# Kernel tuning notes

Measured on AMD Instinct MI355X. Metric: run time of the kernel, lower is better.

Reference implementation:

```python
import jax, jax.numpy as jnp
import numpy as np

N = 50000        # nodes
E = 800000       # directed edges (before self loops)
G = 1024         # graphs in batch
D = 128          # embedding_dim
H = 4            # attention heads
L = 3            # num_layers
NODE_DIM = 78
SLOPE = 0.2      # PyG GATConv leaky_relu negative slope
EPS = 1e-16


def setup_inputs() -> dict:
    key = jax.random.key(0)
    ks = jax.random.split(key, 20)
    s = lambda *sh: 1.0 / np.sqrt(sh[0])
    inp = {
        "x": jax.random.normal(ks[0], (N, NODE_DIM), jnp.float32),
        "edge_index": jax.random.randint(ks[1], (2, E), 0, N, jnp.int64),
        "batch": jnp.sort(jax.random.randint(ks[2], (N,), 0, G, jnp.int64)),
        # node_linear: Linear(78,128) -> ReLU -> Linear(128,128)
        "W1": jax.random.normal(ks[3], (NODE_DIM, D), jnp.float32) * s(NODE_DIM),
        "b1": jnp.zeros((D,), jnp.float32),
        "W2": jax.random.normal(ks[4], (D, D), jnp.float32) * s(D),
        "b2": jnp.zeros((D,), jnp.float32),
        # L stacked GATConv(D, D, heads=H, concat=False)
        "lin_w": jax.random.normal(ks[5], (L, D, H, D), jnp.float32) * s(D),
        "att_src": jax.random.normal(ks[6], (L, H, D), jnp.float32) * s(D),
        "att_dst": jax.random.normal(ks[7], (L, H, D), jnp.float32) * s(D),
        "conv_b": jnp.zeros((L, D), jnp.float32),
        # global_fc: Linear(128,1024) -> ReLU -> Dropout -> Linear(1024,128)
        "gW1": jax.random.normal(ks[8], (D, 1024), jnp.float32) * s(D),
        "gb1": jnp.zeros((1024,), jnp.float32),
        "gW2": jax.random.normal(ks[9], (1024, D), jnp.float32) * s(1024),
        "gb2": jnp.zeros((D,), jnp.float32),
    }
    return inp


def _gat_layer(x, src, dst, W, a_src, a_dst, b):
    # x: [N, D]; W: [D, H, D]
    h = jnp.einsum('nd,dhe->nhe', x, W)                    # [N, H, C]
    a_s = jnp.einsum('nhe,he->nh', h, a_src)               # [N, H]
    a_d = jnp.einsum('nhe,he->nh', h, a_dst)
    e = jax.nn.leaky_relu(a_s[src] + a_d[dst], SLOPE)      # [E', H]
    # segment softmax grouped by destination node
    m = jax.ops.segment_max(e, dst, num_segments=N)
    e = jnp.exp(e - m[dst])
    denom = jax.ops.segment_sum(e, dst, num_segments=N)
    alpha = e / (denom[dst] + EPS)                         # [E', H]
    out = jax.ops.segment_sum(h[src] * alpha[:, :, None], dst, num_segments=N)  # [N, H, C]
    return out.mean(axis=1) + b                            # concat=False: head mean


def reference(x, edge_index, batch, W1, b1, W2, b2, lin_w, att_src, att_dst,
              conv_b, gW1, gb1, gW2, gb2):
    # node_linear MLP
    h = jax.nn.relu(x @ W1 + b1) @ W2 + b2                 # [N, D]
    # add self loops (PyG GATConv default)
    loops = jnp.arange(N, dtype=edge_index.dtype)
    src = jnp.concatenate([edge_index[0], loops])
    dst = jnp.concatenate([edge_index[1], loops])
    for l in range(L):
        h = _gat_layer(h, src, dst, lin_w[l], att_src[l], att_dst[l], conv_b[l])
    # global mean pool per graph
    counts = jax.ops.segment_sum(jnp.ones((N,), h.dtype), batch, num_segments=G)
    pooled = jax.ops.segment_sum(h, batch, num_segments=G) / jnp.maximum(counts, 1.0)[:, None]
    # global_fc (dropout = identity at inference)
    return jax.nn.relu(pooled @ gW1 + gb1) @ gW2 + gb2     # [G, D]
```

## Files before the change

### kernel.cpp

```cpp
#include <hip/hip_runtime.h>
#include <hip/hip_bf16.h>

#define NN 50000
#define EE 800000
#define ET 850000
#define GG 1024
#define DD 128
#define HH 4
#define LL 3
#define ND 78
#define HD 512
#define K1P 96
#define SLOPE 0.2f
#define EPSV 1e-16f
#define SB 196
#define PADS 520

typedef __hip_bfloat16 bf16;
typedef __attribute__((ext_vector_type(8))) unsigned short u16x8;
typedef __attribute__((ext_vector_type(8))) short s16x8;
typedef __attribute__((ext_vector_type(4))) float f32x4;

__device__ __forceinline__ float b2f(bf16 v) { return __bfloat162float(v); }
__device__ __forceinline__ bf16 f2b(float v) { return __float2bfloat16(v); }
__device__ __forceinline__ float bu2f(unsigned short u) {
    return __uint_as_float(((unsigned)u) << 16);
}
__device__ __forceinline__ unsigned short f2bu(float f) {
    unsigned u = __float_as_uint(f);
    unsigned rounded = u + 0x7FFFu + ((u >> 16) & 1u);
    return (unsigned short)(rounded >> 16);
}

__global__ void detect_i(const unsigned* __restrict__ w, int* __restrict__ flag) {
    __shared__ int z;
    int t = threadIdx.x;
    if (t == 0) z = 0;
    __syncthreads();
    if (w[2 * t + 1] == 0u) atomicAdd(&z, 1);
    __syncthreads();
    if (t == 0) flag[0] = (z >= 200) ? 1 : 0;
}
__global__ void conv_i(const void* __restrict__ src, int* __restrict__ dst, int n,
                       const int* __restrict__ flag) {
    int i = blockIdx.x * 256 + threadIdx.x;
    if (i >= n) return;
    const int* s = (const int*)src;
    dst[i] = flag[0] ? s[2 * i] : s[i];
}

__global__ void xconv(const float* __restrict__ x, bf16* __restrict__ xb) {
    int idx = blockIdx.x * 256 + threadIdx.x;
    if (idx >= NN * K1P) return;
    int n = idx / K1P;
    int k = idx % K1P;
    xb[idx] = f2b((k < ND) ? x[(size_t)n * ND + k] : 0.f);
}
__global__ void nw_conv(const float* __restrict__ W1, const float* __restrict__ W2,
                        bf16* __restrict__ W1t, bf16* __restrict__ W2t) {
    int idx = blockIdx.x * 256 + threadIdx.x;
    if (idx < DD * K1P) {
        int c = idx / K1P, k = idx % K1P;
        W1t[idx] = f2b((k < ND) ? W1[(size_t)k * DD + c] : 0.f);
    }
    idx -= DD * K1P;
    if (idx >= 0 && idx < DD * DD) {
        int c = idx / DD, k = idx % DD;
        W2t[idx] = f2b(W2[(size_t)k * DD + c]);
    }
}

__global__ __launch_bounds__(256) void mlp_gemm1(const bf16* __restrict__ xb,
                                                 const bf16* __restrict__ W1t,
                                                 const float* __restrict__ b1,
                                                 bf16* __restrict__ ts) {
    int wid = (blockIdx.x * 256 + threadIdx.x) >> 6;
    if (wid >= NN / 16) return;
    int lane = threadIdx.x & 63;
    int r16 = lane & 15;
    int q = lane >> 4;
    const short* ab = (const short*)xb;
    const short* bb = (const short*)W1t;
    int arow = wid * 16 + r16;
    s16x8 afr[3];
#pragma unroll
    for (int c = 0; c < 3; c++) afr[c] = *(const s16x8*)(ab + (size_t)arow * K1P + c * 32 + q * 8);
#pragma unroll
    for (int nt = 0; nt < 8; nt++) {
        int brow = nt * 16 + r16;
        f32x4 acc = {0.f, 0.f, 0.f, 0.f};
#pragma unroll
        for (int c = 0; c < 3; c++) {
            s16x8 b = *(const s16x8*)(bb + (size_t)brow * K1P + c * 32 + q * 8);
            acc = __builtin_amdgcn_mfma_f32_16x16x32_bf16(afr[c], b, acc, 0, 0, 0);
        }
        int cc = nt * 16 + r16;
        float bias = b1[cc];
#pragma unroll
        for (int r = 0; r < 4; r++) {
            int row = wid * 16 + q * 4 + r;
            ts[(size_t)row * DD + cc] = f2b(fmaxf(acc[r] + bias, 0.f));
        }
    }
}

__global__ __launch_bounds__(256) void mlp_gemm2(const bf16* __restrict__ ts,
                                                 const bf16* __restrict__ W2t,
                                                 const float* __restrict__ b2,
                                                 bf16* __restrict__ h) {
    int wid = (blockIdx.x * 256 + threadIdx.x) >> 6;
    if (wid >= NN / 16) return;
    int lane = threadIdx.x & 63;
    int r16 = lane & 15;
    int q = lane >> 4;
    const short* ab = (const short*)ts;
    const short* bb = (const short*)W2t;
    int arow = wid * 16 + r16;
    s16x8 afr[4];
#pragma unroll
    for (int c = 0; c < 4; c++) afr[c] = *(const s16x8*)(ab + (size_t)arow * DD + c * 32 + q * 8);
#pragma unroll
    for (int nt = 0; nt < 8; nt++) {
        int brow = nt * 16 + r16;
        f32x4 acc = {0.f, 0.f, 0.f, 0.f};
#pragma unroll
        for (int c = 0; c < 4; c++) {
            s16x8 b = *(const s16x8*)(bb + (size_t)brow * DD + c * 32 + q * 8);
            acc = __builtin_amdgcn_mfma_f32_16x16x32_bf16(afr[c], b, acc, 0, 0, 0);
        }
        int cc = nt * 16 + r16;
        float bias = b2[cc];
#pragma unroll
        for (int r = 0; r < 4; r++) {
            int row = wid * 16 + q * 4 + r;
            h[(size_t)row * DD + cc] = f2b(acc[r] + bias);
        }
    }
}

__global__ void init_deg(int* deg) {
    int n = blockIdx.x * 256 + threadIdx.x;
    if (n < NN) deg[n] = 1;
}
__global__ void hist_edges(const int* __restrict__ ei, int* deg) {
    int e = blockIdx.x * 256 + threadIdx.x;
    if (e >= EE) return;
    int dst = ei[EE + e];
    if ((unsigned)dst < NN) atomicAdd(&deg[dst], 1);
}
__global__ __launch_bounds__(256) void block_sums(const int* __restrict__ deg, int* __restrict__ bsum) {
    __shared__ int part[256];
    int t = threadIdx.x;
    int i = blockIdx.x * 256 + t;
    part[t] = (i < NN) ? deg[i] : 0;
    __syncthreads();
    for (int off = 128; off > 0; off >>= 1) {
        if (t < off) part[t] += part[t + off];
        __syncthreads();
    }
    if (t == 0) bsum[blockIdx.x] = part[0];
}
__global__ __launch_bounds__(256) void scan_bsum(const int* __restrict__ bsum, int* __restrict__ boff,
                                                 int* __restrict__ start) {
    __shared__ int part[256];
    int t = threadIdx.x;
    part[t] = (t < SB) ? bsum[t] : 0;
    __syncthreads();
    for (int off = 1; off < 256; off <<= 1) {
        int add = (t >= off) ? part[t - off] : 0;
        __syncthreads();
        part[t] += add;
        __syncthreads();
    }
    if (t < SB) boff[t] = (t == 0) ? 0 : part[t - 1];
    if (t == 255) start[NN] = part[SB - 1];
}
__global__ __launch_bounds__(256) void scan_final(const int* __restrict__ deg, const int* __restrict__ boff,
                                                  int* __restrict__ start, int* __restrict__ cursor) {
    __shared__ int part[256];
    int t = threadIdx.x;
    int i = blockIdx.x * 256 + t;
    int v = (i < NN) ? deg[i] : 0;
    part[t] = v;
    __syncthreads();
    for (int off = 1; off < 256; off <<= 1) {
        int add = (t >= off) ? part[t - off] : 0;
        __syncthreads();
        part[t] += add;
        __syncthreads();
    }
    if (i < NN) {
        int ex = boff[blockIdx.x] + part[t] - v;
        start[i] = ex;
        cursor[i] = ex;
    }
}
__global__ void scatter_self(int* cursor, int* ssrc) {
    int n = blockIdx.x * 256 + threadIdx.x;
    if (n >= NN) return;
    int pos = atomicAdd(&cursor[n], 1);
    if ((unsigned)pos < ET) ssrc[pos] = n;
}
__global__ void scatter_edges(const int* __restrict__ ei, int* cursor, int* ssrc) {
    int e = blockIdx.x * 256 + threadIdx.x;
    if (e >= EE) return;
    int src = ei[e];
    int dst = ei[EE + e];
    if ((unsigned)dst >= NN) return;
    int pos = atomicAdd(&cursor[dst], 1);
    if ((unsigned)pos < ET) ssrc[pos] = ((unsigned)src < NN) ? src : 0;
}

__global__ void asd_w(const float* __restrict__ lin_w, const float* __restrict__ att_src,
                      const float* __restrict__ att_dst,
                      float* __restrict__ ws, float* __restrict__ wd) {
    int idx = blockIdx.x * 256 + threadIdx.x;
    if (idx >= LL * DD * HH) return;
    int l = idx / (DD * HH);
    int rem = idx % (DD * HH);
    int d = rem >> 2;
    int h = rem & 3;
    const float* wrow = lin_w + ((size_t)(l * DD + d) * HH + h) * DD;
    const float* as = att_src + (size_t)(l * HH + h) * DD;
    const float* ad = att_dst + (size_t)(l * HH + h) * DD;
    float s1 = 0.f, s2 = 0.f;
    for (int e = 0; e < DD; e++) { float w = wrow[e]; s1 += w * as[e]; s2 += w * ad[e]; }
    ws[idx] = s1;
    wd[idx] = s2;
}

__global__ void wt2_conv(const float* __restrict__ lin_w, bf16* __restrict__ Bt) {
    int idx = blockIdx.x * 256 + threadIdx.x;
    if (idx >= LL * DD * HD) return;
    int l = idx / (DD * HD);
    int rem = idx % (DD * HD);
    int c = rem / HD;
    int k = rem % HD;
    int h = k >> 7;
    int d = k & 127;
    Bt[idx] = f2b(lin_w[((size_t)(l * DD + d) * HH + h) * DD + c]);
}

__global__ void gw_conv(const float* __restrict__ gW1, const float* __restrict__ gW2,
                        bf16* __restrict__ gW1t, bf16* __restrict__ gW2t) {
    int idx = blockIdx.x * 256 + threadIdx.x;
    if (idx < 1024 * DD) {
        int c = idx / DD, k = idx % DD;
        gW1t[idx] = f2b(gW1[(size_t)k * 1024 + c]);
    }
    idx -= 1024 * DD;
    if (idx >= 0 && idx < DD * 1024) {
        int c = idx / 1024, k = idx % 1024;
        gW2t[idx] = f2b(gW2[(size_t)k * DD + c]);
    }
}

__global__ __launch_bounds__(256) void a_sd2(const bf16* __restrict__ h,
                                             const float* __restrict__ ws,
                                             const float* __restrict__ wd,
                                             float* __restrict__ a_s, float* __restrict__ a_d) {
    __shared__ float wsl[DD][HH];
    __shared__ float wdl[DD][HH];
    int t = threadIdx.x;
    for (int i = t; i < DD * HH; i += 256) { wsl[i >> 2][i & 3] = ws[i]; wdl[i >> 2][i & 3] = wd[i]; }
    __syncthreads();
    int n = blockIdx.x * 256 + t;
    if (n >= NN) return;
    const u16x8* row = (const u16x8*)((const unsigned short*)h + (size_t)n * DD);
    float s1[HH] = {0.f, 0.f, 0.f, 0.f};
    float s2[HH] = {0.f, 0.f, 0.f, 0.f};
    for (int c = 0; c < 16; c++) {
        u16x8 v = row[c];
#pragma unroll
        for (int k = 0; k < 8; k++) {
            int d = c * 8 + k;
            float f = bu2f(v[k]);
#pragma unroll
            for (int hh = 0; hh < HH; hh++) {
                s1[hh] += f * wsl[d][hh];
                s2[hh] += f * wdl[d][hh];
            }
        }
    }
#pragma unroll
    for (int hh = 0; hh < HH; hh++) {
        a_s[n * HH + hh] = s1[hh];
        a_d[n * HH + hh] = s2[hh];
    }
}

__global__ __launch_bounds__(256) void edge_weights(const int* __restrict__ start,
                                                    const int* __restrict__ ssrc,
                                                    const float* __restrict__ a_s,
                                                    const float* __restrict__ a_d,
                                                    float* __restrict__ w,
                                                    float* __restrict__ invbuf) {
    int node = (blockIdx.x * 256 + threadIdx.x) >> 6;
    if (node >= NN) return;
    int lane = threadIdx.x & 63;
    int jj = lane & 15;
    int h = lane >> 4;
    int s0 = start[node];
    int deg = start[node + 1] - s0;
    float ad = a_d[node * HH + h];
    float ec[4];
    float mx = -1e30f;
#pragma unroll
    for (int k = 0; k < 4; k++) {
        int j = jj + k * 16;
        float e = -1e30f;
        if (j < deg) {
            int s = ssrc[s0 + j];
            e = a_s[s * HH + h] + ad;
            e = (e > 0.f) ? e : SLOPE * e;
        }
        ec[k] = e;
        mx = fmaxf(mx, e);
    }
    for (int j = jj + 64; j < deg; j += 16) {
        int s = ssrc[s0 + j];
        float e = a_s[s * HH + h] + ad;
        e = (e > 0.f) ? e : SLOPE * e;
        mx = fmaxf(mx, e);
    }
#pragma unroll
    for (int off = 1; off < 16; off <<= 1) mx = fmaxf(mx, __shfl_xor(mx, off));
    float den = 0.f;
#pragma unroll
    for (int k = 0; k < 4; k++) {
        int j = jj + k * 16;
        if (j < deg) {
            float ww = __expf(ec[k] - mx);
            den += ww;
            w[(size_t)(s0 + j) * HH + h] = ww;
        }
    }
    for (int j = jj + 64; j < deg; j += 16) {
        int s = ssrc[s0 + j];
        float e = a_s[s * HH + h] + ad;
        e = (e > 0.f) ? e : SLOPE * e;
        float ww = __expf(e - mx);
        den += ww;
        w[(size_t)(s0 + j) * HH + h] = ww;
    }
#pragma unroll
    for (int off = 1; off < 16; off <<= 1) den += __shfl_xor(den, off);
    if (jj == 0) invbuf[node * HH + h] = 1.f / (den + EPSV);
}

__global__ __launch_bounds__(1024) void agg_gemm(const int* __restrict__ start,
                                                 const int* __restrict__ ssrc,
                                                 const float* __restrict__ w,
                                                 const float* __restrict__ invbuf,
                                                 const bf16* __restrict__ h,
                                                 const bf16* __restrict__ Bt,
                                                 const float* __restrict__ conv_b,
                                                 bf16* __restrict__ hnext) {
    __shared__ short aggL[16 * PADS];
    int wv = threadIdx.x >> 6;
    int lane = threadIdx.x & 63;
    int node16 = blockIdx.x * 16;
    int node = node16 + wv;

    int s0 = start[node];
    int deg = start[node + 1] - s0;
    const unsigned* hu = (const unsigned*)h;
    float acc[HH][2];
#pragma unroll
    for (int hh = 0; hh < HH; hh++) { acc[hh][0] = 0.f; acc[hh][1] = 0.f; }

    auto fmaEdge = [&](float4 w4, unsigned hv) {
        float v0 = bu2f((unsigned short)(hv & 0xFFFFu));
        float v1 = bu2f((unsigned short)(hv >> 16));
        acc[0][0] += w4.x * v0; acc[0][1] += w4.x * v1;
        acc[1][0] += w4.y * v0; acc[1][1] += w4.y * v1;
        acc[2][0] += w4.z * v0; acc[2][1] += w4.z * v1;
        acc[3][0] += w4.w * v0; acc[3][1] += w4.w * v1;
    };

    int j = 0;
    for (; j + 4 <= deg; j += 4) {
        int e0 = s0 + j;
        int sA = ssrc[e0], sB = ssrc[e0 + 1], sC = ssrc[e0 + 2], sD = ssrc[e0 + 3];
        float4 wA = *(const float4*)(w + (size_t)e0 * HH);
        float4 wB = *(const float4*)(w + (size_t)(e0 + 1) * HH);
        float4 wC = *(const float4*)(w + (size_t)(e0 + 2) * HH);
        float4 wD = *(const float4*)(w + (size_t)(e0 + 3) * HH);
        unsigned hA = hu[(size_t)sA * (DD / 2) + lane];
        unsigned hB = hu[(size_t)sB * (DD / 2) + lane];
        unsigned hC = hu[(size_t)sC * (DD / 2) + lane];
        unsigned hD = hu[(size_t)sD * (DD / 2) + lane];
        fmaEdge(wA, hA);
        fmaEdge(wB, hB);
        fmaEdge(wC, hC);
        fmaEdge(wD, hD);
    }
    for (; j < deg; j++) {
        int e0 = s0 + j;
        int s = ssrc[e0];
        float4 w4 = *(const float4*)(w + (size_t)e0 * HH);
        unsigned hv = hu[(size_t)s * (DD / 2) + lane];
        fmaEdge(w4, hv);
    }
    float4 inv4 = *(const float4*)(invbuf + node * HH);
    float invs[HH] = {inv4.x, inv4.y, inv4.z, inv4.w};
    unsigned* aggU = (unsigned*)aggL;
#pragma unroll
    for (int hh = 0; hh < HH; hh++) {
        unsigned packed = (unsigned)f2bu(acc[hh][0] * invs[hh]) |
                          ((unsigned)f2bu(acc[hh][1] * invs[hh]) << 16);
        aggU[wv * (PADS / 2) + hh * (DD / 2) + lane] = packed;
    }
    __syncthreads();

    if (wv < 8) {
        int nt = wv;
        int r16 = lane & 15;
        int q = lane >> 4;
        const short* bb = (const short*)Bt;
        int brow = nt * 16 + r16;
        f32x4 gacc = {0.f, 0.f, 0.f, 0.f};
#pragma unroll
        for (int c = 0; c < 16; c++) {
            s16x8 a = *(const s16x8*)(aggL + r16 * PADS + c * 32 + q * 8);
            s16x8 b = *(const s16x8*)(bb + (size_t)brow * HD + c * 32 + q * 8);
            gacc = __builtin_amdgcn_mfma_f32_16x16x32_bf16(a, b, gacc, 0, 0, 0);
        }
        int cc = nt * 16 + r16;
        float bias = conv_b[cc];
#pragma unroll
        for (int r = 0; r < 4; r++) {
            int row = node16 + q * 4 + r;
            hnext[(size_t)row * DD + cc] = f2b(0.25f * gacc[r] + bias);
        }
    }
}

__global__ void pool_init(float* pooled, int* counts) {
    int idx = blockIdx.x * 256 + threadIdx.x;
    if (idx < GG * DD) pooled[idx] = 0.f;
    if (idx < GG) counts[idx] = 0;
}
__global__ void pool_count(const int* __restrict__ batch, int* counts) {
    int n = blockIdx.x * 256 + threadIdx.x;
    if (n >= NN) return;
    int g = batch[n];
    if ((unsigned)g < GG) atomicAdd(&counts[g], 1);
}
__global__ __launch_bounds__(256) void pool_accum2(const bf16* __restrict__ h,
                                                   const int* __restrict__ batch,
                                                   float* pooled) {
    int t = threadIdx.x;
    int d = t & 127;
    int half = t >> 7;
    int n0 = blockIdx.x * 64 + half * 32;
    int n1 = n0 + 32; if (n1 > NN) n1 = NN;
    float acc = 0.f;
    int cur = -1;
    for (int n = n0; n < n1; n++) {
        int g = batch[n];
        if ((unsigned)g >= GG) continue;
        if (g != cur) {
            if (cur >= 0) atomicAdd(&pooled[cur * DD + d], acc);
            acc = 0.f; cur = g;
        }
        acc += b2f(h[(size_t)n * DD + d]);
    }
    if (cur >= 0) atomicAdd(&pooled[cur * DD + d], acc);
}
__global__ void pooled2bf(const float* __restrict__ pooled, const int* __restrict__ counts,
                          bf16* __restrict__ pbf) {
    int idx = blockIdx.x * 256 + threadIdx.x;
    if (idx >= GG * DD) return;
    int g = idx >> 7;
    int c = counts[g]; if (c < 1) c = 1;
    pbf[idx] = f2b(pooled[idx] / (float)c);
}

__global__ __launch_bounds__(256) void fc1_mfma(const bf16* __restrict__ pbf,
                                                const bf16* __restrict__ gW1t,
                                                const float* __restrict__ gb1,
                                                bf16* __restrict__ t1) {
    int wid = (blockIdx.x * 256 + threadIdx.x) >> 6;
    int lane = threadIdx.x & 63;
    int mt = wid >> 6;
    int nt = wid & 63;
    int r16 = lane & 15;
    int q = lane >> 4;
    const short* ab = (const short*)pbf;
    const short* bb = (const short*)gW1t;
    f32x4 acc = {0.f, 0.f, 0.f, 0.f};
    int arow = mt * 16 + r16;
    int brow = nt * 16 + r16;
#pragma unroll
    for (int c = 0; c < 4; c++) {
        s16x8 a = *(const s16x8*)(ab + (size_t)arow * DD + c * 32 + q * 8);
        s16x8 b = *(const s16x8*)(bb + (size_t)brow * DD + c * 32 + q * 8);
        acc = __builtin_amdgcn_mfma_f32_16x16x32_bf16(a, b, acc, 0, 0, 0);
    }
    int cc = nt * 16 + r16;
    float bias = gb1[cc];
#pragma unroll
    for (int r = 0; r < 4; r++) {
        int row = mt * 16 + q * 4 + r;
        t1[(size_t)row * 1024 + cc] = f2b(fmaxf(acc[r] + bias, 0.f));
    }
}

__global__ __launch_bounds__(256) void fc2_mfma(const bf16* __restrict__ t1,
                                                const bf16* __restrict__ gW2t,
                                                const float* __restrict__ gb2,
                                                float* __restrict__ out) {
    int wid = (blockIdx.x * 256 + threadIdx.x) >> 6;
    int lane = threadIdx.x & 63;
    int mt = wid >> 3;
    int nt = wid & 7;
    int r16 = lane & 15;
    int q = lane >> 4;
    const short* ab = (const short*)t1;
    const short* bb = (const short*)gW2t;
    f32x4 acc = {0.f, 0.f, 0.f, 0.f};
    int arow = mt * 16 + r16;
    int brow = nt * 16 + r16;
#pragma unroll
    for (int c = 0; c < 32; c++) {
        s16x8 a = *(const s16x8*)(ab + (size_t)arow * 1024 + c * 32 + q * 8);
        s16x8 b = *(const s16x8*)(bb + (size_t)brow * 1024 + c * 32 + q * 8);
        acc = __builtin_amdgcn_mfma_f32_16x16x32_bf16(a, b, acc, 0, 0, 0);
    }
    int cc = nt * 16 + r16;
    float bias = gb2[cc];
#pragma unroll
    for (int r = 0; r < 4; r++) {
        int row = mt * 16 + q * 4 + r;
        out[(size_t)row * DD + cc] = acc[r] + bias;
    }
}

__global__ void init_checks(int* nanbad) {
    if (threadIdx.x == 0 && blockIdx.x == 0) nanbad[0] = 0;
}
__global__ void nan_check(const bf16* __restrict__ h, int* bad) {
    int i = blockIdx.x * 256 + threadIdx.x;
    if (i >= NN * DD) return;
    float v = b2f(h[i]);
    if (v != v || fabsf(v) > 1e30f) bad[0] = 1;
}
__global__ void sentinel(float* out, const int* __restrict__ start, const int* __restrict__ nanbad) {
    if (threadIdx.x != 0 || blockIdx.x != 0) return;
    int code = 0;
    if (start[NN] != ET) code = 31000;
    else if (nanbad[0]) code = 33000;
    if (code) out[0] = (float)code;
}
__global__ void sentinel_only(float* out, int hostcode) {
    if (threadIdx.x == 0 && blockIdx.x == 0) out[0] = (float)hostcode;
}

extern "C" void kernel_launch(void* const* d_in, const int* in_sizes, int n_in,
                              void* d_out, int out_size, void* d_ws, size_t ws_size,
                              hipStream_t stream) {
    float* out = (float*)d_out;

    static const int expect[15] = {3900000, 1600000, 50000, 9984, 128, 16384, 128,
                                   196608, 1536, 1536, 384, 131072, 1024, 131072, 128};
    int hostcode = 0;
    if (n_in != 15) hostcode = 21099;
    else for (int i = 0; i < 15; i++) if (in_sizes[i] != expect[i]) { hostcode = 21000 + i; break; }
    if (hostcode == 0 && out_size != GG * DD) hostcode = 35000;

    const float* x       = (const float*)d_in[0];
    const float* W1      = (const float*)d_in[3];
    const float* b1      = (const float*)d_in[4];
    const float* W2      = (const float*)d_in[5];
    const float* b2      = (const float*)d_in[6];
    const float* lin_w   = (const float*)d_in[7];
    const float* att_src = (const float*)d_in[8];
    const float* att_dst = (const float*)d_in[9];
    const float* conv_b  = (const float*)d_in[10];
    const float* gW1     = (const float*)d_in[11];
    const float* gb1     = (const float*)d_in[12];
    const float* gW2     = (const float*)d_in[13];
    const float* gb2     = (const float*)d_in[14];

    char* p = (char*)d_ws;
    auto alloc = [&](size_t bytes) { void* q = (void*)p; p += (bytes + 255) & ~(size_t)255; return q; };
    int*   flags  = (int*)alloc(4 * 4);
    int*   nanbad = (int*)alloc(4);
    int*   ei32   = (int*)alloc((size_t)2 * EE * 4);
    int*   bat32  = (int*)alloc((size_t)NN * 4);
    bf16*  xb     = (bf16*)alloc((size_t)NN * K1P * 2);
    bf16*  W1tb   = (bf16*)alloc((size_t)DD * K1P * 2);
    bf16*  W2tb   = (bf16*)alloc((size_t)DD * DD * 2);
    bf16*  tsbuf  = (bf16*)alloc((size_t)NN * DD * 2);
    bf16*  hA     = (bf16*)alloc((size_t)NN * DD * 2);
    bf16*  hB     = (bf16*)alloc((size_t)NN * DD * 2);
    bf16*  Bt     = (bf16*)alloc((size_t)LL * DD * HD * 2);
    float* wsbuf  = (float*)alloc((size_t)LL * DD * HH * 4);
    float* wdbuf  = (float*)alloc((size_t)LL * DD * HH * 4);
    float* a_s    = (float*)alloc((size_t)NN * HH * 4);
    float* a_d    = (float*)alloc((size_t)NN * HH * 4);
    float* wbuf   = (float*)alloc((size_t)ET * HH * 4);
    float* invbuf = (float*)alloc((size_t)NN * HH * 4);
    int*   deg    = (int*)alloc((size_t)NN * 4);
    int*   start  = (int*)alloc((size_t)(NN + 1) * 4);
    int*   cursor = (int*)alloc((size_t)NN * 4);
    int*   ssrc   = (int*)alloc((size_t)ET * 4);
    int*   bsum   = (int*)alloc((size_t)SB * 4);
    int*   boff   = (int*)alloc((size_t)SB * 4);
    float* pooled = (float*)alloc((size_t)GG * DD * 4);
    int*   counts = (int*)alloc((size_t)GG * 4);
    bf16*  pbf    = (bf16*)alloc((size_t)GG * DD * 2);
    bf16*  gW1t   = (bf16*)alloc((size_t)1024 * DD * 2);
    bf16*  gW2t   = (bf16*)alloc((size_t)DD * 1024 * 2);
    bf16*  t1buf  = (bf16*)alloc((size_t)GG * 1024 * 2);
    size_t need = (size_t)(p - (char*)d_ws);
    if (hostcode == 0 && ws_size < need) hostcode = 34000;

    if (hostcode != 0) {
        sentinel_only<<<1, 64, 0, stream>>>(out, hostcode);
        return;
    }

    detect_i<<<1, 256, 0, stream>>>((const unsigned*)d_in[1], flags + 0);
    detect_i<<<1, 256, 0, stream>>>((const unsigned*)d_in[2], flags + 1);
    conv_i<<<(2 * EE + 255) / 256, 256, 0, stream>>>(d_in[1], ei32, 2 * EE, flags + 0);
    conv_i<<<(NN + 255) / 256, 256, 0, stream>>>(d_in[2], bat32, NN, flags + 1);

    xconv<<<((size_t)NN * K1P + 255) / 256, 256, 0, stream>>>(x, xb);
    nw_conv<<<(DD * K1P + DD * DD + 255) / 256, 256, 0, stream>>>(W1, W2, W1tb, W2tb);
    mlp_gemm1<<<(NN / 16 * 64 + 255) / 256, 256, 0, stream>>>(xb, W1tb, b1, tsbuf);
    mlp_gemm2<<<(NN / 16 * 64 + 255) / 256, 256, 0, stream>>>(tsbuf, W2tb, b2, hA);

    asd_w<<<(LL * DD * HH + 255) / 256, 256, 0, stream>>>(lin_w, att_src, att_dst, wsbuf, wdbuf);
    wt2_conv<<<(LL * DD * HD + 255) / 256, 256, 0, stream>>>(lin_w, Bt);
    gw_conv<<<(2 * 1024 * DD + 255) / 256, 256, 0, stream>>>(gW1, gW2, gW1t, gW2t);
    init_deg<<<(NN + 255) / 256, 256, 0, stream>>>(deg);
    hist_edges<<<(EE + 255) / 256, 256, 0, stream>>>(ei32, deg);
    block_sums<<<SB, 256, 0, stream>>>(deg, bsum);
    scan_bsum<<<1, 256, 0, stream>>>(bsum, boff, start);
    scan_final<<<SB, 256, 0, stream>>>(deg, boff, start, cursor);
    scatter_self<<<(NN + 255) / 256, 256, 0, stream>>>(cursor, ssrc);
    scatter_edges<<<(EE + 255) / 256, 256, 0, stream>>>(ei32, cursor, ssrc);

    const int NWB = (NN * 64 + 255) / 256;
    bf16* hin = hA;
    bf16* hout = hB;
    for (int l = 0; l < LL; l++) {
        a_sd2<<<(NN + 255) / 256, 256, 0, stream>>>(hin, wsbuf + l * DD * HH, wdbuf + l * DD * HH, a_s, a_d);
        edge_weights<<<NWB, 256, 0, stream>>>(start, ssrc, a_s, a_d, wbuf, invbuf);
        agg_gemm<<<NN / 16, 1024, 0, stream>>>(start, ssrc, wbuf, invbuf, hin,
                                               Bt + (size_t)l * DD * HD, conv_b + l * DD, hout);
        bf16* tmp = hin; hin = hout; hout = tmp;
    }
    pool_init<<<(GG * DD + 255) / 256, 256, 0, stream>>>(pooled, counts);
    pool_count<<<(NN + 255) / 256, 256, 0, stream>>>(bat32, counts);
    pool_accum2<<<(NN + 63) / 64, 256, 0, stream>>>(hin, bat32, pooled);
    pooled2bf<<<(GG * DD + 255) / 256, 256, 0, stream>>>(pooled, counts, pbf);
    fc1_mfma<<<(64 * 64) / 4, 256, 0, stream>>>(pbf, gW1t, gb1, t1buf);
    fc2_mfma<<<(64 * 8) / 4, 256, 0, stream>>>(t1buf, gW2t, gb2, out);

    init_checks<<<1, 64, 0, stream>>>(nanbad);
    nan_check<<<((size_t)NN * DD + 255) / 256, 256, 0, stream>>>(hin, nanbad);
    sentinel<<<1, 64, 0, stream>>>(out, start, nanbad);
}
```

Before: 685.8 us.

## Fuse edge softmax weights into aggregation kernel and drop debug checks

Merges the edge_weights kernel into the aggregation+GEMM kernel. Each wave now computes its node's softmax weights in 64-edge chunks into LDS and consumes them directly, so the global edge-weight and inverse-denominator buffers are no longer written and re-read. It also removes the NaN check and sentinel kernels at the end. The fused kernel uses more LDS per block and recomputes logits for high-degree nodes, which may lower occupancy.

```diff
diff --git a/kernel.cpp b/kernel.cpp
--- a/kernel.cpp
+++ b/kernel.cpp
@@ -289,20 +289,28 @@
     }
 }
 
-__global__ __launch_bounds__(256) void edge_weights(const int* __restrict__ start,
-                                                    const int* __restrict__ ssrc,
-                                                    const float* __restrict__ a_s,
-                                                    const float* __restrict__ a_d,
-                                                    float* __restrict__ w,
-                                                    float* __restrict__ invbuf) {
-    int node = (blockIdx.x * 256 + threadIdx.x) >> 6;
-    if (node >= NN) return;
+__global__ __launch_bounds__(1024) void gat_layer(const int* __restrict__ start,
+                                                  const int* __restrict__ ssrc,
+                                                  const float* __restrict__ a_s,
+                                                  const float* __restrict__ a_d,
+                                                  const bf16* __restrict__ h,
+                                                  const bf16* __restrict__ Bt,
+                                                  const float* __restrict__ conv_b,
+                                                  bf16* __restrict__ hnext) {
+    __shared__ short aggL[16 * PADS];
+    __shared__ float wL[16][64][HH];
+    __shared__ float invL[16][HH];
+    int wv = threadIdx.x >> 6;
     int lane = threadIdx.x & 63;
-    int jj = lane & 15;
-    int h = lane >> 4;
+    int node16 = blockIdx.x * 16;
+    int node = node16 + wv;
     int s0 = start[node];
     int deg = start[node + 1] - s0;
-    float ad = a_d[node * HH + h];
+
+    int jj = lane & 15;
+    int hh4 = lane >> 4;
+    float ad = a_d[node * HH + hh4];
+
     float ec[4];
     float mx = -1e30f;
 #pragma unroll
@@ -311,7 +319,7 @@
         float e = -1e30f;
         if (j < deg) {
             int s = ssrc[s0 + j];
-            e = a_s[s * HH + h] + ad;
+            e = a_s[s * HH + hh4] + ad;
             e = (e > 0.f) ? e : SLOPE * e;
         }
         ec[k] = e;
@@ -319,55 +327,18 @@
     }
     for (int j = jj + 64; j < deg; j += 16) {
         int s = ssrc[s0 + j];
-        float e = a_s[s * HH + h] + ad;
+        float e = a_s[s * HH + hh4] + ad;
         e = (e > 0.f) ? e : SLOPE * e;
         mx = fmaxf(mx, e);
     }
 #pragma unroll
     for (int off = 1; off < 16; off <<= 1) mx = fmaxf(mx, __shfl_xor(mx, off));
+
     float den = 0.f;
-#pragma unroll
-    for (int k = 0; k < 4; k++) {
-        int j = jj + k * 16;
-        if (j < deg) {
-            float ww = __expf(ec[k] - mx);
-            den += ww;
-            w[(size_t)(s0 + j) * HH + h] = ww;
-        }
-    }
-    for (int j = jj + 64; j < deg; j += 16) {
-        int s = ssrc[s0 + j];
-        float e = a_s[s * HH + h] + ad;
-        e = (e > 0.f) ? e : SLOPE * e;
-        float ww = __expf(e - mx);
-        den += ww;
-        w[(size_t)(s0 + j) * HH + h] = ww;
-    }
-#pragma unroll
-    for (int off = 1; off < 16; off <<= 1) den += __shfl_xor(den, off);
-    if (jj == 0) invbuf[node * HH + h] = 1.f / (den + EPSV);
-}
-
-__global__ __launch_bounds__(1024) void agg_gemm(const int* __restrict__ start,
-                                                 const int* __restrict__ ssrc,
-                                                 const float* __restrict__ w,
-                                                 const float* __restrict__ invbuf,
-                                                 const bf16* __restrict__ h,
-                                                 const bf16* __restrict__ Bt,
-                                                 const float* __restrict__ conv_b,
-                                                 bf16* __restrict__ hnext) {
-    __shared__ short aggL[16 * PADS];
-    int wv = threadIdx.x >> 6;
-    int lane = threadIdx.x & 63;
-    int node16 = blockIdx.x * 16;
-    int node = node16 + wv;
-
-    int s0 = start[node];
-    int deg = start[node + 1] - s0;
+    float acc[HH][2];
+#pragma unroll
+    for (int hh = 0; hh < HH; hh++) { acc[hh][0] = 0.f; acc[hh][1] = 0.f; }
     const unsigned* hu = (const unsigned*)h;
-    float acc[HH][2];
-#pragma unroll
-    for (int hh = 0; hh < HH; hh++) { acc[hh][0] = 0.f; acc[hh][1] = 0.f; }
 
     auto fmaEdge = [&](float4 w4, unsigned hv) {
         float v0 = bu2f((unsigned short)(hv & 0xFFFFu));
@@ -378,31 +349,61 @@
         acc[3][0] += w4.w * v0; acc[3][1] += w4.w * v1;
     };
 
-    int j = 0;
-    for (; j + 4 <= deg; j += 4) {
-        int e0 = s0 + j;
-        int sA = ssrc[e0], sB = ssrc[e0 + 1], sC = ssrc[e0 + 2], sD = ssrc[e0 + 3];
-        float4 wA = *(const float4*)(w + (size_t)e0 * HH);
-        float4 wB = *(const float4*)(w + (size_t)(e0 + 1) * HH);
-        float4 wC = *(const float4*)(w + (size_t)(e0 + 2) * HH);
-        float4 wD = *(const float4*)(w + (size_t)(e0 + 3) * HH);
-        unsigned hA = hu[(size_t)sA * (DD / 2) + lane];
-        unsigned hB = hu[(size_t)sB * (DD / 2) + lane];
-        unsigned hC = hu[(size_t)sC * (DD / 2) + lane];
-        unsigned hD = hu[(size_t)sD * (DD / 2) + lane];
-        fmaEdge(wA, hA);
-        fmaEdge(wB, hB);
-        fmaEdge(wC, hC);
-        fmaEdge(wD, hD);
-    }
-    for (; j < deg; j++) {
-        int e0 = s0 + j;
-        int s = ssrc[e0];
-        float4 w4 = *(const float4*)(w + (size_t)e0 * HH);
-        unsigned hv = hu[(size_t)s * (DD / 2) + lane];
-        fmaEdge(w4, hv);
-    }
-    float4 inv4 = *(const float4*)(invbuf + node * HH);
+    for (int c0 = 0; c0 < deg; c0 += 64) {
+        int m = deg - c0; if (m > 64) m = 64;
+        if (c0 == 0) {
+#pragma unroll
+            for (int k = 0; k < 4; k++) {
+                int j = jj + k * 16;
+                if (j < m) {
+                    float w = __expf(ec[k] - mx);
+                    den += w;
+                    wL[wv][j][hh4] = w;
+                }
+            }
+        } else {
+            for (int j = jj; j < m; j += 16) {
+                int s = ssrc[s0 + c0 + j];
+                float e = a_s[s * HH + hh4] + ad;
+                e = (e > 0.f) ? e : SLOPE * e;
+                float w = __expf(e - mx);
+                den += w;
+                wL[wv][j][hh4] = w;
+            }
+        }
+        __builtin_amdgcn_wave_barrier();
+        int j = 0;
+        for (; j + 4 <= m; j += 4) {
+            int e0 = s0 + c0 + j;
+            int sA = ssrc[e0], sB = ssrc[e0 + 1], sC = ssrc[e0 + 2], sD = ssrc[e0 + 3];
+            float4 wA = *(const float4*)&wL[wv][j][0];
+            float4 wB = *(const float4*)&wL[wv][j + 1][0];
+            float4 wC = *(const float4*)&wL[wv][j + 2][0];
+            float4 wD = *(const float4*)&wL[wv][j + 3][0];
+            unsigned hA = hu[(size_t)sA * (DD / 2) + lane];
+            unsigned hB = hu[(size_t)sB * (DD / 2) + lane];
+            unsigned hC = hu[(size_t)sC * (DD / 2) + lane];
+            unsigned hD = hu[(size_t)sD * (DD / 2) + lane];
+            fmaEdge(wA, hA);
+            fmaEdge(wB, hB);
+            fmaEdge(wC, hC);
+            fmaEdge(wD, hD);
+        }
+        for (; j < m; j++) {
+            int e0 = s0 + c0 + j;
+            int s = ssrc[e0];
+            float4 w4 = *(const float4*)&wL[wv][j][0];
+            unsigned hv = hu[(size_t)s * (DD / 2) + lane];
+            fmaEdge(w4, hv);
+        }
+        __builtin_amdgcn_wave_barrier();
+    }
+
+#pragma unroll
+    for (int off = 1; off < 16; off <<= 1) den += __shfl_xor(den, off);
+    if (jj == 0) invL[wv][hh4] = 1.f / (den + EPSV);
+    __builtin_amdgcn_wave_barrier();
+    float4 inv4 = *(const float4*)&invL[wv][0];
     float invs[HH] = {inv4.x, inv4.y, inv4.z, inv4.w};
     unsigned* aggU = (unsigned*)aggL;
 #pragma unroll
@@ -537,22 +538,6 @@
     }
 }
 
-__global__ void init_checks(int* nanbad) {
-    if (threadIdx.x == 0 && blockIdx.x == 0) nanbad[0] = 0;
-}
-__global__ void nan_check(const bf16* __restrict__ h, int* bad) {
-    int i = blockIdx.x * 256 + threadIdx.x;
-    if (i >= NN * DD) return;
-    float v = b2f(h[i]);
-    if (v != v || fabsf(v) > 1e30f) bad[0] = 1;
-}
-__global__ void sentinel(float* out, const int* __restrict__ start, const int* __restrict__ nanbad) {
-    if (threadIdx.x != 0 || blockIdx.x != 0) return;
-    int code = 0;
-    if (start[NN] != ET) code = 31000;
-    else if (nanbad[0]) code = 33000;
-    if (code) out[0] = (float)code;
-}
 __global__ void sentinel_only(float* out, int hostcode) {
     if (threadIdx.x == 0 && blockIdx.x == 0) out[0] = (float)hostcode;
 }
@@ -586,7 +571,6 @@
     char* p = (char*)d_ws;
     auto alloc = [&](size_t bytes) { void* q = (void*)p; p += (bytes + 255) & ~(size_t)255; return q; };
     int*   flags  = (int*)alloc(4 * 4);
-    int*   nanbad = (int*)alloc(4);
     int*   ei32   = (int*)alloc((size_t)2 * EE * 4);
     int*   bat32  = (int*)alloc((size_t)NN * 4);
     bf16*  xb     = (bf16*)alloc((size_t)NN * K1P * 2);
@@ -600,8 +584,6 @@
     float* wdbuf  = (float*)alloc((size_t)LL * DD * HH * 4);
     float* a_s    = (float*)alloc((size_t)NN * HH * 4);
     float* a_d    = (float*)alloc((size_t)NN * HH * 4);
-    float* wbuf   = (float*)alloc((size_t)ET * HH * 4);
-    float* invbuf = (float*)alloc((size_t)NN * HH * 4);
     int*   deg    = (int*)alloc((size_t)NN * 4);
     int*   start  = (int*)alloc((size_t)(NN + 1) * 4);
     int*   cursor = (int*)alloc((size_t)NN * 4);
@@ -643,14 +625,12 @@
     scatter_self<<<(NN + 255) / 256, 256, 0, stream>>>(cursor, ssrc);
     scatter_edges<<<(EE + 255) / 256, 256, 0, stream>>>(ei32, cursor, ssrc);
 
-    const int NWB = (NN * 64 + 255) / 256;
     bf16* hin = hA;
     bf16* hout = hB;
     for (int l = 0; l < LL; l++) {
         a_sd2<<<(NN + 255) / 256, 256, 0, stream>>>(hin, wsbuf + l * DD * HH, wdbuf + l * DD * HH, a_s, a_d);
-        edge_weights<<<NWB, 256, 0, stream>>>(start, ssrc, a_s, a_d, wbuf, invbuf);
-        agg_gemm<<<NN / 16, 1024, 0, stream>>>(start, ssrc, wbuf, invbuf, hin,
-                                               Bt + (size_t)l * DD * HD, conv_b + l * DD, hout);
+        gat_layer<<<NN / 16, 1024, 0, stream>>>(start, ssrc, a_s, a_d, hin,
+                                                Bt + (size_t)l * DD * HD, conv_b + l * DD, hout);
         bf16* tmp = hin; hin = hout; hout = tmp;
     }
     pool_init<<<(GG * DD + 255) / 256, 256, 0, stream>>>(pooled, counts);
@@ -659,8 +639,4 @@
     pooled2bf<<<(GG * DD + 255) / 256, 256, 0, stream>>>(pooled, counts, pbf);
     fc1_mfma<<<(64 * 64) / 4, 256, 0, stream>>>(pbf, gW1t, gb1, t1buf);
     fc2_mfma<<<(64 * 8) / 4, 256, 0, stream>>>(t1buf, gW2t, gb2, out);
-
-    init_checks<<<1, 64, 0, stream>>>(nanbad);
-    nan_check<<<((size_t)NN * DD + 255) / 256, 256, 0, stream>>>(hin, nanbad);
-    sentinel<<<1, 64, 0, stream>>>(out, start, nanbad);
-}
+}
```

Result: slower. 739.0 us (+7.8%).
